# Kernel tuning notes

Measured on AMD Instinct MI355X. Metric: run time of the kernel, lower is better.

The kernel has to match this reference:

```python
import jax, jax.numpy as jnp
import numpy as np
from jax import lax

# Module config (mirrors init_kwargs)
N, CIN, COUT, H, W = 16, 512, 512, 64, 64
KS = 3          # conv kernel_size
FACTOR = 2
GAIN = 1.0
LRMUL = 1.0
FIR_1D = np.array([1.0, 3.0, 3.0, 1.0], dtype=np.float32)

# upfirdn pad amounts as in the torch code
FIRN = 4
P = FIRN - FACTOR + (KS - 1)      # = 4
PAD0 = (P + 1) // 2               # = 2
PAD1 = P // 2                     # = 2
W_LRMUL = GAIN / np.sqrt(CIN * COUT * KS * KS)  # he_std * lrmul (use_wscale)
B_LRMUL = LRMUL
SQRT2 = np.float32(np.sqrt(2.0))


def setup_inputs() -> dict:
    key = jax.random.key(0)
    kx, kw, kb = jax.random.split(key, 3)
    x = jax.random.normal(kx, (N, CIN, H, W), dtype=jnp.float32)
    # weight init: randn * init_std, init_std = 1/lrmul = 1.0 under use_wscale
    weight = jax.random.normal(kw, (COUT, CIN, KS, KS), dtype=jnp.float32)
    bias = jax.random.normal(kb, (COUT,), dtype=jnp.float32) * 0.1
    kf = np.outer(FIR_1D, FIR_1D)
    kf = kf / kf.sum() * GAIN
    fir = jnp.asarray(kf, dtype=jnp.float32)  # [4,4], non-trainable
    return {"x": x, "weight": weight, "bias": bias, "fir": fir}


def _blur_and_resize(x, fir):
    # x: [N, C, H, W]; FIR blur via depthwise trick: fold C into batch.
    n, c, h, w = x.shape
    y = x.reshape(n * c, 1, h, w)
    y = jnp.pad(y, ((0, 0), (0, 0), (PAD0, PAD1), (PAD0, PAD1)))
    # valid conv with 4x4 FIR -> [n*c, 1, h+1, w+1]
    y = lax.conv_general_dilated(
        y, fir[None, None, :, :], window_strides=(1, 1), padding="VALID",
        dimension_numbers=("NCHW", "OIHW", "NCHW"))
    # F.interpolate(mode='nearest') from (h+1, w+1) back to (h, w):
    # torch nearest uses src = floor(dst * in/out) == (dst*(h+1))//h
    ri = (jnp.arange(h) * (h + 1)) // h
    ci = (jnp.arange(w) * (w + 1)) // w
    y = y[:, :, ri, :][:, :, :, ci]
    return y.reshape(n, c, h, w)


def reference(x, weight, bias, fir):
    y = _blur_and_resize(x, fir)
    # strided conv: stride=factor, padding=ks//2 (SAME-ish), cross-correlation
    out = lax.conv_general_dilated(
        y, weight * W_LRMUL, window_strides=(FACTOR, FACTOR),
        padding=[(KS // 2, KS // 2), (KS // 2, KS // 2)],
        dimension_numbers=("NCHW", "OIHW", "NCHW"))
    out = out + (bias * B_LRMUL)[None, :, None, None]
    out = jnp.where(out >= 0, out, 0.2 * out) * SQRT2  # leaky_relu(0.2) * sqrt(2)
    return out
```

## Files before the change

### kernel.cpp

```cpp
#include <hip/hip_runtime.h>
#include <hip/hip_bf16.h>
#include <stdint.h>

#define N_IMG 16
#define C_IN  512
#define C_OUT 512
#define H_IN  64
#define W_IN  64
#define OH    32
#define OW    32
#define PIX   (N_IMG*OH*OW)

#define YPH 65
#define YPW 33

#define W2_ELEMS (9*C_OUT*C_IN)
#define W2_BYTES (W2_ELEMS*2)

#define BM 128
#define BN 256
#define BK 64
#define NKT 72
#define ATILE_B (BM*BK*2)
#define BTILE_B (BN*BK*2)
#define BUF_B   (ATILE_B+BTILE_B)
#define LDS_TOTAL (3*BUF_B)

typedef __attribute__((ext_vector_type(8))) __bf16 bf16x8;
typedef __attribute__((ext_vector_type(4))) float  f32x4;

__device__ inline void gload_lds16(const void* g, void* l) {
  __builtin_amdgcn_global_load_lds(
      (const __attribute__((address_space(1))) void*)g,
      (__attribute__((address_space(3))) void*)l, 16, 0, 0);
}

#define WAIT_VM(N) asm volatile("s_waitcnt vmcnt(" #N ")" ::: "memory")
__device__ inline void barrier_raw() {
  asm volatile("" ::: "memory");
  __builtin_amdgcn_s_barrier();
  asm volatile("" ::: "memory");
}

struct TagMain  { static constexpr bool stg = true;  static constexpr int vn = 6;  };
struct TagTail0 { static constexpr bool stg = false; static constexpr int vn = 0;  };
struct TagTail1 { static constexpr bool stg = false; static constexpr int vn = -1; };

__global__ __launch_bounds__(256) void prep_w_kernel(const float* __restrict__ w,
                                                     __hip_bfloat16* __restrict__ w2) {
  int id = blockIdx.x * 256 + threadIdx.x;
  const float* p = w + (size_t)id * 9;
  float v[9];
#pragma unroll
  for (int t = 0; t < 9; ++t) v[t] = p[t] * (1.0f/1536.0f);
#pragma unroll
  for (int t = 0; t < 9; ++t)
    w2[(size_t)t*(C_OUT*C_IN) + id] = __float2bfloat16(v[t]);
}

__global__ __launch_bounds__(512, 4) void blur_kernel(const float* __restrict__ x,
                                                      __hip_bfloat16* __restrict__ yt) {
  __shared__ float obuf[2][64][65];
  const int tid = threadIdx.x;
  const int c   = tid >> 3;
  const int p8  = tid & 7;
  const int w8  = p8 * 8;
  const int r0  = blockIdx.x * 16;
  const int cc  = blockIdx.y;
  const int n   = blockIdx.z;
  const float* xc = x + ((size_t)(n*C_IN + cc*64 + c) * H_IN) * W_IN + w8;

  {
    const uint4 z4 = {0u, 0u, 0u, 0u};
    if (tid < 256) {
      int idx = tid >> 3;
      int ci8 = tid & 7;
      int hh  = r0 + (idx >> 1);
      int par = idx & 1;
      size_t slot = (((size_t)n*YPH + hh + 1)*2 + par)*YPW;
      *(uint4*)(yt + slot*C_IN + cc*64 + ci8*8) = z4;
    }
    if (blockIdx.x == 0) {
#pragma unroll
      for (int i = 0; i < 2; ++i) {
        int id = i*512 + tid;
        if (id < 528) {
          int si  = id >> 3;
          int c8  = id & 7;
          int par = (si >= 33) ? 1 : 0;
          int wq  = si - par*33;
          size_t slot = (((size_t)n*YPH)*2 + par)*YPW + wq;
          *(uint4*)(yt + slot*C_IN + cc*64 + c8*8) = z4;
        }
      }
    }
  }

  const int rp_ci8 = tid & 7;
  const int rp_p   = tid >> 3;

  float cur[8], nxt[8], nx2[8];
  float h1[8], h2[8], h3[8];
#pragma unroll
  for (int j = 0; j < 8; ++j) { h1[j] = 0.f; h2[j] = 0.f; h3[j] = 0.f; }

  auto load_row = [&](int r, float* dst) {
    if (r >= 0 && r < H_IN) {
      const float4 a = *(const float4*)(xc + (size_t)r * W_IN);
      const float4 b = *(const float4*)(xc + (size_t)r * W_IN + 4);
      dst[0]=a.x; dst[1]=a.y; dst[2]=a.z; dst[3]=a.w;
      dst[4]=b.x; dst[5]=b.y; dst[6]=b.z; dst[7]=b.w;
    } else {
#pragma unroll
      for (int j = 0; j < 8; ++j) dst[j] = 0.f;
    }
  };

  load_row(r0 - 2, cur);
  load_row(r0 - 1, nxt);
#pragma unroll
  for (int ri = 0; ri < 19; ++ri) {
    const int r = r0 - 2 + ri;
    if (ri < 17) load_row(r + 2, nx2);

    float l2 = __shfl_up(cur[6], 1);
    float l1 = __shfl_up(cur[7], 1);
    float rr = __shfl_down(cur[0], 1);
    if (p8 == 0) { l2 = 0.f; l1 = 0.f; }
    if (p8 == 7) { rr = 0.f; }
    float hc[8];
    hc[0] = l2 + 3.f*(l1 + cur[0]) + cur[1];
    hc[1] = l1 + 3.f*(cur[0] + cur[1]) + cur[2];
#pragma unroll
    for (int j = 2; j < 7; ++j) hc[j] = cur[j-2] + 3.f*(cur[j-1] + cur[j]) + cur[j+1];
    hc[7] = cur[5] + 3.f*(cur[6] + cur[7]) + rr;

    if (ri >= 3) {
      const int h = r - 1;
      const int b = ri & 1;
#pragma unroll
      for (int j = 0; j < 8; ++j)
        obuf[b][c][w8 + j] = (h3[j] + 3.f*(h2[j] + h1[j]) + hc[j]) * (1.0f/64.0f);
      __syncthreads();
      alignas(16) __hip_bfloat16 t16[8];
#pragma unroll
      for (int j = 0; j < 8; ++j)
        t16[j] = __float2bfloat16(obuf[b][rp_ci8*8 + j][rp_p]);
      size_t slot = ((size_t)(n*YPH + h + 1)*2 + (rp_p & 1))*YPW + (rp_p >> 1) + 1;
      *(uint4*)(yt + slot*C_IN + cc*64 + rp_ci8*8) = *(uint4*)t16;
    }

#pragma unroll
    for (int j = 0; j < 8; ++j) {
      h3[j] = h2[j]; h2[j] = h1[j]; h1[j] = hc[j]; cur[j] = nxt[j]; nxt[j] = nx2[j];
    }
  }
}

__global__ __launch_bounds__(512, 2) void conv_kernel(const __hip_bfloat16* __restrict__ w2,
                            const __hip_bfloat16* __restrict__ yt,
                            const float* __restrict__ bias,
                            float* __restrict__ out) {
  extern __shared__ char lds[];
  const int tid   = threadIdx.x;
  const int lane  = tid & 63;
  const int wv    = tid >> 6;
  const int wvb64 = wv * 64;
  const int wm    = wv & 1;
  const int wn    = wv >> 1;
  const int cob0  = blockIdx.y * BM;
  const int pixb  = blockIdx.x * BN;
  const int quad  = lane >> 4;

  size_t aoff[2];
#pragma unroll
  for (int i = 0; i < 2; ++i) {
    int s = i*512 + tid, r = s >> 3, p = s & 7, g = p ^ (r & 7);
    aoff[i] = (size_t)(cob0 + r)*C_IN + g*8;
  }
  int bn65[4], boh2[4], bow_[4], bseg8[4];
#pragma unroll
  for (int i = 0; i < 4; ++i) {
    int s = i*512 + tid, r = s >> 3, p = s & 7, g = p ^ (r & 7);
    int gp = pixb + r;
    bn65[i]  = (gp >> 10) * YPH;
    boh2[i]  = ((gp >> 5) & 31) * 2;
    bow_[i]  = gp & 31;
    bseg8[i] = g*8;
  }

  int aRdOff[4][2], bRdOff[4][2];
#pragma unroll
  for (int f = 0; f < 4; ++f) {
    int ra = wm*64 + f*16 + (lane & 15);
    int rb = wn*64 + f*16 + (lane & 15);
#pragma unroll
    for (int kk = 0; kk < 2; ++kk) {
      aRdOff[f][kk] = ra*128 + (((kk*4 + quad) ^ (ra & 7)) * 16);
      bRdOff[f][kk] = rb*128 + (((kk*4 + quad) ^ (rb & 7)) * 16);
    }
  }

  struct BP { int kh, par, d, cib; };
  auto bparams = [&](int kt) {
    const int t  = kt >> 3;
    const int kh = (t * 11) >> 5;
    const int kw = t - kh*3;
    BP r; r.kh = kh; r.par = (kw == 1) ? 0 : 1; r.d = (kw == 0) ? 0 : 1;
    r.cib = (kt & 7) << 6;
    return r;
  };
  auto stageTile = [&](int kt, int b) {
    const int t = kt >> 3;
    const __hip_bfloat16* wt = w2 + (size_t)t*(C_OUT*C_IN) + ((kt & 7) << 6);
    char* da = lds + b*BUF_B;
    gload_lds16(wt + aoff[0], da + (size_t)(      wvb64)*16);
    gload_lds16(wt + aoff[1], da + (size_t)(512 + wvb64)*16);
    BP bp = bparams(kt);
    char* db = da + ATILE_B;
#pragma unroll
    for (int i = 0; i < 4; ++i) {
      size_t s = ((size_t)(bn65[i] + boh2[i] + bp.kh)*2 + bp.par)*YPW + bow_[i] + bp.d;
      gload_lds16(yt + s*C_IN + bseg8[i] + bp.cib, db + (size_t)(i*512 + wvb64)*16);
    }
  };

  f32x4 acc[4][4];
  const f32x4 zero = {0.f, 0.f, 0.f, 0.f};
#pragma unroll
  for (int mi = 0; mi < 4; ++mi)
#pragma unroll
    for (int ni = 0; ni < 4; ++ni) acc[mi][ni] = zero;

  stageTile(0, 0);
  stageTile(1, 1);
  WAIT_VM(6);
  barrier_raw();

  auto body = [&](int k, int cb, int sb, auto tag) {
    using T = decltype(tag);
    const char* Ab = lds + cb*BUF_B;
    const char* Bb = Ab + ATILE_B;

    bf16x8 af[4][2], bfv[4][2];
#pragma unroll
    for (int mi = 0; mi < 4; ++mi)
#pragma unroll
      for (int kk = 0; kk < 2; ++kk)
        af[mi][kk] = *(const bf16x8*)(Ab + aRdOff[mi][kk]);
#pragma unroll
    for (int ni = 0; ni < 4; ++ni)
#pragma unroll
      for (int kk = 0; kk < 2; ++kk)
        bfv[ni][kk] = *(const bf16x8*)(Bb + bRdOff[ni][kk]);

    if constexpr (T::stg) stageTile(k + 2, sb);

    __builtin_amdgcn_s_setprio(1);
#pragma unroll
    for (int kk = 0; kk < 2; ++kk)
#pragma unroll
      for (int mi = 0; mi < 4; ++mi)
#pragma unroll
        for (int ni = 0; ni < 4; ++ni)
          acc[mi][ni] = __builtin_amdgcn_mfma_f32_16x16x32_bf16(af[mi][kk], bfv[ni][kk], acc[mi][ni], 0, 0, 0);
    __builtin_amdgcn_s_setprio(0);

    if constexpr (T::vn == 6) WAIT_VM(6);
    else if constexpr (T::vn == 0) WAIT_VM(0);
    barrier_raw();
  };

  int cb = 0, sb = 2;
  for (int k = 0; k < NKT - 2; ++k) {
    body(k, cb, sb, TagMain{});
    cb = (cb == 2) ? 0 : cb + 1;
    sb = (sb == 2) ? 0 : sb + 1;
  }
  body(NKT - 2, cb, sb, TagTail0{});
  cb = (cb == 2) ? 0 : cb + 1;
  body(NKT - 1, cb, 0, TagTail1{});

#pragma unroll
  for (int mi = 0; mi < 4; ++mi) {
#pragma unroll
    for (int reg = 0; reg < 4; ++reg) {
      int co = cob0 + wm*64 + mi*16 + quad*4 + reg;
      float bv = bias[co];
#pragma unroll
      for (int ni = 0; ni < 4; ++ni) {
        int gp  = pixb + wn*64 + ni*16 + (lane & 15);
        int n   = gp >> 10;
        int ohw = gp & 1023;
        float v = acc[mi][ni][reg] + bv;
        v = (v >= 0.f ? v : 0.2f*v) * 1.41421356f;
        out[(((size_t)n*C_OUT + co) << 10) + ohw] = v;
      }
    }
  }
}

extern "C" void kernel_launch(void* const* d_in, const int* in_sizes, int n_in,
                              void* d_out, int out_size, void* d_ws, size_t ws_size,
                              hipStream_t stream) {
  const float* x    = (const float*)d_in[0];
  const float* w    = (const float*)d_in[1];
  const float* bias = (const float*)d_in[2];
  float* out = (float*)d_out;
  __hip_bfloat16* w2 = (__hip_bfloat16*)d_ws;
  __hip_bfloat16* yt = (__hip_bfloat16*)((char*)d_ws + W2_BYTES);

  static bool attr_set = false;
  if (!attr_set) {
    hipFuncSetAttribute(reinterpret_cast<const void*>(conv_kernel),
                        hipFuncAttributeMaxDynamicSharedMemorySize, LDS_TOTAL);
    attr_set = true;
  }

  prep_w_kernel<<<(C_OUT*C_IN)/256, 256, 0, stream>>>(w, w2);
  blur_kernel<<<dim3(4, 8, 16), 512, 0, stream>>>(x, yt);
  conv_kernel<<<dim3(PIX/BN, C_OUT/BM), 512, LDS_TOTAL, stream>>>(w2, yt, bias, out);
}
```

Before: 306.3 us.

## Load weight fragments directly from global memory instead of staging through LDS

Removes the weight (A) tile from the LDS staging pipeline, so each wave reads its bf16 weight fragments straight from global memory into registers at the start of every k-step. Only the activation (B) tile is still triple-buffered through LDS, which cuts LDS footprint and the async-load count per stage. The vmcnt wait values are adjusted to match, and sched_barriers fence the B staging. The cost is that global-load latency for A now sits on the critical path of each iteration with no prefetch. The four waves sharing a row block also fetch the same weight data redundantly.

```diff
diff --git a/kernel.cpp b/kernel.cpp
--- a/kernel.cpp
+++ b/kernel.cpp
@@ -21,9 +21,7 @@
 #define BN 256
 #define BK 64
 #define NKT 72
-#define ATILE_B (BM*BK*2)
-#define BTILE_B (BN*BK*2)
-#define BUF_B   (ATILE_B+BTILE_B)
+#define BUF_B (BN*BK*2)
 #define LDS_TOTAL (3*BUF_B)
 
 typedef __attribute__((ext_vector_type(8))) __bf16 bf16x8;
@@ -36,13 +34,14 @@
 }
 
 #define WAIT_VM(N) asm volatile("s_waitcnt vmcnt(" #N ")" ::: "memory")
+#define WAIT_LGKM0 asm volatile("s_waitcnt lgkmcnt(0)" ::: "memory")
 __device__ inline void barrier_raw() {
   asm volatile("" ::: "memory");
   __builtin_amdgcn_s_barrier();
   asm volatile("" ::: "memory");
 }
 
-struct TagMain  { static constexpr bool stg = true;  static constexpr int vn = 6;  };
+struct TagMain  { static constexpr bool stg = true;  static constexpr int vn = 4;  };
 struct TagTail0 { static constexpr bool stg = false; static constexpr int vn = 0;  };
 struct TagTail1 { static constexpr bool stg = false; static constexpr int vn = -1; };
 
@@ -172,12 +171,6 @@
   const int pixb  = blockIdx.x * BN;
   const int quad  = lane >> 4;
 
-  size_t aoff[2];
-#pragma unroll
-  for (int i = 0; i < 2; ++i) {
-    int s = i*512 + tid, r = s >> 3, p = s & 7, g = p ^ (r & 7);
-    aoff[i] = (size_t)(cob0 + r)*C_IN + g*8;
-  }
   int bn65[4], boh2[4], bow_[4], bseg8[4];
 #pragma unroll
   for (int i = 0; i < 4; ++i) {
@@ -189,17 +182,19 @@
     bseg8[i] = g*8;
   }
 
-  int aRdOff[4][2], bRdOff[4][2];
+  size_t arow[4];
+#pragma unroll
+  for (int mi = 0; mi < 4; ++mi)
+    arow[mi] = (size_t)(cob0 + wm*64 + mi*16 + (lane & 15)) * C_IN;
+  int bRdOff[4][2];
 #pragma unroll
   for (int f = 0; f < 4; ++f) {
-    int ra = wm*64 + f*16 + (lane & 15);
     int rb = wn*64 + f*16 + (lane & 15);
 #pragma unroll
-    for (int kk = 0; kk < 2; ++kk) {
-      aRdOff[f][kk] = ra*128 + (((kk*4 + quad) ^ (ra & 7)) * 16);
+    for (int kk = 0; kk < 2; ++kk)
       bRdOff[f][kk] = rb*128 + (((kk*4 + quad) ^ (rb & 7)) * 16);
-    }
-  }
+  }
+  const int kq8[2] = { quad*8, (4 + quad)*8 };
 
   struct BP { int kh, par, d, cib; };
   auto bparams = [&](int kt) {
@@ -210,14 +205,9 @@
     r.cib = (kt & 7) << 6;
     return r;
   };
-  auto stageTile = [&](int kt, int b) {
-    const int t = kt >> 3;
-    const __hip_bfloat16* wt = w2 + (size_t)t*(C_OUT*C_IN) + ((kt & 7) << 6);
-    char* da = lds + b*BUF_B;
-    gload_lds16(wt + aoff[0], da + (size_t)(      wvb64)*16);
-    gload_lds16(wt + aoff[1], da + (size_t)(512 + wvb64)*16);
+  auto stageB = [&](int kt, int b) {
     BP bp = bparams(kt);
-    char* db = da + ATILE_B;
+    char* db = lds + b*BUF_B;
 #pragma unroll
     for (int i = 0; i < 4; ++i) {
       size_t s = ((size_t)(bn65[i] + boh2[i] + bp.kh)*2 + bp.par)*YPW + bow_[i] + bp.d;
@@ -232,29 +222,35 @@
 #pragma unroll
     for (int ni = 0; ni < 4; ++ni) acc[mi][ni] = zero;
 
-  stageTile(0, 0);
-  stageTile(1, 1);
-  WAIT_VM(6);
+  stageB(0, 0);
+  stageB(1, 1);
+  WAIT_VM(4);
   barrier_raw();
 
   auto body = [&](int k, int cb, int sb, auto tag) {
     using T = decltype(tag);
-    const char* Ab = lds + cb*BUF_B;
-    const char* Bb = Ab + ATILE_B;
-
-    bf16x8 af[4][2], bfv[4][2];
+    const char* Bb = lds + cb*BUF_B;
+    const int t   = k >> 3;
+    const int cib = (k & 7) << 6;
+    const __hip_bfloat16* wt = w2 + (size_t)t*(C_OUT*C_IN) + cib;
+
+    bf16x8 af[4][2];
 #pragma unroll
     for (int mi = 0; mi < 4; ++mi)
 #pragma unroll
       for (int kk = 0; kk < 2; ++kk)
-        af[mi][kk] = *(const bf16x8*)(Ab + aRdOff[mi][kk]);
+        af[mi][kk] = *(const bf16x8*)(wt + arow[mi] + kq8[kk]);
+
+    bf16x8 bfv[4][2];
 #pragma unroll
     for (int ni = 0; ni < 4; ++ni)
 #pragma unroll
       for (int kk = 0; kk < 2; ++kk)
         bfv[ni][kk] = *(const bf16x8*)(Bb + bRdOff[ni][kk]);
 
-    if constexpr (T::stg) stageTile(k + 2, sb);
+    __builtin_amdgcn_sched_barrier(0);
+    if constexpr (T::stg) stageB(k + 2, sb);
+    __builtin_amdgcn_sched_barrier(0);
 
     __builtin_amdgcn_s_setprio(1);
 #pragma unroll
@@ -266,9 +262,8 @@
           acc[mi][ni] = __builtin_amdgcn_mfma_f32_16x16x32_bf16(af[mi][kk], bfv[ni][kk], acc[mi][ni], 0, 0, 0);
     __builtin_amdgcn_s_setprio(0);
 
-    if constexpr (T::vn == 6) WAIT_VM(6);
-    else if constexpr (T::vn == 0) WAIT_VM(0);
-    barrier_raw();
+    if constexpr (T::vn == 4) { WAIT_VM(4); barrier_raw(); }
+    else if constexpr (T::vn == 0) { WAIT_VM(0); barrier_raw(); }
   };
 
   int cb = 0, sb = 2;
```

Result: slower. 418.3 us (+36.6%).
